# Performance work log

Hardware: AMD Instinct MI355X
Metric: run time of the kernel (lower is better)

Reference implementation:

```python
import jax, jax.numpy as jnp
import numpy as np

G = 64          # grid_size
BC = 16         # base_channels
LATENT = 128

def _conv3d_s2(x, w, b):
    # x: [B,C,D,H,W], w: [O,I,3,3,3], stride 2, pad 1
    y = jax.lax.conv_general_dilated(
        x, w, window_strides=(2, 2, 2), padding=((1, 1), (1, 1), (1, 1)),
        dimension_numbers=('NCDHW', 'OIDHW', 'NCDHW'))
    return y + b[None, :, None, None, None]

def setup_inputs() -> dict:
    key = jax.random.key(0)
    ks = jax.random.split(key, 9)
    B, N = 32, 16384
    partial_coords = jax.random.uniform(ks[0], (B, N, 3), jnp.float32, -1.0, 1.0)
    def he(k, shape, fan_in):
        return jax.random.normal(k, shape, jnp.float32) * np.float32(np.sqrt(2.0 / fan_in))
    w1 = he(ks[1], (BC, 1, 3, 3, 3), 1 * 27)
    b1 = jnp.zeros((BC,), jnp.float32)
    w2 = he(ks[2], (2 * BC, BC, 3, 3, 3), BC * 27)
    b2 = jnp.zeros((2 * BC,), jnp.float32)
    w3 = he(ks[3], (4 * BC, 2 * BC, 3, 3, 3), 2 * BC * 27)
    b3 = jnp.zeros((4 * BC,), jnp.float32)
    fc_in = 4 * BC * (G // 8) ** 3
    fc_w = he(ks[4], (LATENT, fc_in), fc_in)
    fc_b = jnp.zeros((LATENT,), jnp.float32)
    return {'partial_coords': partial_coords, 'w1': w1, 'b1': b1, 'w2': w2,
            'b2': b2, 'w3': w3, 'b3': b3, 'fc_w': fc_w, 'fc_b': fc_b}

def reference(partial_coords, w1, b1, w2, b2, w3, b3, fc_w, fc_b):
    B, N, _ = partial_coords.shape
    # voxelize: scale [-1,1] -> [0, G-1], truncate (matches torch .long()), clamp
    coords_scaled = (partial_coords + 1.0) * 0.5 * (G - 1)
    ci = jnp.clip(coords_scaled.astype(jnp.int32), 0, G - 1)  # [B,N,3] = (x,y,z)
    bidx = jnp.broadcast_to(jnp.arange(B, dtype=jnp.int32)[:, None], (B, N))
    grid = jnp.zeros((B, G, G, G), jnp.float32)
    # grid[b, z, y, x] = 1.0  (single vectorized scatter)
    grid = grid.at[bidx, ci[..., 2], ci[..., 1], ci[..., 0]].set(1.0)
    x = grid[:, None]  # [B,1,G,G,G]
    x = jax.nn.relu(_conv3d_s2(x, w1, b1))
    x = jax.nn.relu(_conv3d_s2(x, w2, b2))
    x = jax.nn.relu(_conv3d_s2(x, w3, b3))  # [B,4*BC,G/8,G/8,G/8]
    feat = x.reshape(B, -1)
    return feat @ fc_w.T + fc_b  # [B,128]
```

## Files before the change

kernel.cpp:

```cpp
#include <hip/hip_runtime.h>
#include <hip/hip_bf16.h>


typedef __attribute__((ext_vector_type(8))) short bf16x8;
typedef __attribute__((ext_vector_type(4))) float f32x4;

__device__ inline unsigned short f2bf(float f) {
    __hip_bfloat16 h = __float2bfloat16(f);
    return *reinterpret_cast<unsigned short*>(&h);
}

__global__ void k_scatter(const float* __restrict__ coords,
                          unsigned char* __restrict__ grid) {
    int i = blockIdx.x * 256 + threadIdx.x;
    float cx = coords[3 * i + 0];
    float cy = coords[3 * i + 1];
    float cz = coords[3 * i + 2];
    int ix = (int)((cx + 1.0f) * 0.5f * 63.0f);
    int iy = (int)((cy + 1.0f) * 0.5f * 63.0f);
    int iz = (int)((cz + 1.0f) * 0.5f * 63.0f);
    ix = min(max(ix, 0), 63);
    iy = min(max(iy, 0), 63);
    iz = min(max(iz, 0), 63);
    int b = i >> 14;
    grid[((b * 64 + iz) * 64 + iy) * 64 + ix] = 1;
}

__global__ __launch_bounds__(256) void k_conv1(
        const unsigned char* __restrict__ grid,
        const float* __restrict__ w1,
        const float* __restrict__ b1,
        unsigned short* __restrict__ c1b) {
    __shared__ float hal[9 * 17 * 20];
    const int t = threadIdx.x;
    const int blk = blockIdx.x;
    const int b = blk >> 7;
    const int zb = (blk >> 4) & 7;
    const int yb = (blk >> 2) & 3;
    const int xb = blk & 3;
    const int iz0 = 8 * zb - 1, iy0 = 16 * yb - 1, ix0 = 16 * xb - 1;

    const unsigned char* g = grid + b * 262144;
    for (int i = t; i < 2601; i += 256) {
        int hz = i / 289, rm = i - hz * 289;
        int hy = rm / 17, hx = rm - hy * 17;
        int iz = iz0 + hz, iy = iy0 + hy, ix = ix0 + hx;
        bool ok = (iz >= 0) & (iy >= 0) & (ix >= 0);
        float v = ok ? (float)g[(iz * 64 + iy) * 64 + ix] : 0.0f;
        int ux = (hx & 1) ? 10 + (hx >> 1) : (hx >> 1);
        hal[(hz * 17 + hy) * 20 + ux] = v;
    }
    __syncthreads();

    const int x = t & 7, y = (t >> 3) & 7, tz = t >> 6;
    const int base = (2 * tz * 17) * 20 + (2 * y) * 20 + x;
    float in27[27];
#pragma unroll
    for (int kz = 0; kz < 3; ++kz)
#pragma unroll
        for (int ky = 0; ky < 3; ++ky)
#pragma unroll
            for (int kx = 0; kx < 3; ++kx) {
                int uxo = (kx == 1) ? 10 : ((kx == 2) ? 1 : 0);
                in27[kz * 9 + ky * 3 + kx] =
                    hal[base + (kz * 17 + ky) * 20 + uxo];
            }
    float r[16];
#pragma unroll
    for (int oc = 0; oc < 16; ++oc) {
        float acc = b1[oc];
#pragma unroll
        for (int k = 0; k < 27; ++k) acc = fmaf(w1[oc * 27 + k], in27[k], acc);
        r[oc] = fmaxf(acc, 0.0f);
    }
    unsigned int dw[8];
#pragma unroll
    for (int j = 0; j < 8; ++j)
        dw[j] = (unsigned int)f2bf(r[2 * j]) | ((unsigned int)f2bf(r[2 * j + 1]) << 16);
    int oz = 4 * zb + tz, oy = 8 * yb + y, ox = 8 * xb + x;
    size_t idx = ((size_t)(b * 32 + oz) * 32 + oy) * 32 + ox;
    char* base_o = (char*)c1b + idx * 32;
    *(int4*)base_o        = int4{(int)dw[0], (int)dw[1], (int)dw[2], (int)dw[3]};
    *(int4*)(base_o + 16) = int4{(int)dw[4], (int)dw[5], (int)dw[6], (int)dw[7]};
}

__global__ void k_wtrans(const float* __restrict__ w2, unsigned short* __restrict__ w2b,
                         const float* __restrict__ w3, unsigned short* __restrict__ w3b) {
    int i = blockIdx.x * 256 + threadIdx.x;
    if (i < 14336) {
        int sh = i >> 9, oc = (i >> 4) & 31, c = i & 15;
        float v = (sh < 27) ? w2[oc * 432 + c * 27 + sh] : 0.0f;
        w2b[i] = f2bf(v);
    } else {
        int j = i - 14336;
        if (j < 55296) {
            int sh = j >> 11, oc = (j >> 5) & 63, c = j & 31;
            w3b[j] = f2bf(w3[oc * 864 + c * 27 + sh]);
        }
    }
}

__device__ constexpr int abase(int sh) {
    return (sh / 9) * 35376 + (((sh % 9) / 3) & 1) * 18224 +
           (((sh % 9) / 3) >> 1) * 1072 + (sh % 3) * 32;
}

__global__ __launch_bounds__(512) void k_conv2_mfma(
        const unsigned short* __restrict__ c1b,
        const unsigned short* __restrict__ w2b,
        const float* __restrict__ b2,
        unsigned short* __restrict__ c2b) {
    __shared__ __align__(16) char smem[106128];
    const int t = threadIdx.x;
    const int b = blockIdx.x >> 4;
    const int zo = blockIdx.x & 15;
    const int lane = t & 63;
    const int wid = t >> 6;

    {
        const int4 z4 = {0, 0, 0, 0};
        if (t < 198) {
            int p = t / 66, r = t % 66;
            int col = r >> 1, h = r & 1;
            *(int4*)(smem + p * 35376 + col * 32 + h * 16) = z4;
        }
        if (t >= 256 && t < 454) {
            int i = t - 256;
            int p = i / 66, r = i % 66;
            int row33 = r >> 1, h = r & 1;
            int off = (row33 < 17) ? row33 * 1072 : 18224 + (row33 - 17) * 1072;
            *(int4*)(smem + p * 35376 + off + h * 16) = z4;
        }
    }

    const char* src = (const char*)c1b + (size_t)b * (32768 * 32);
#pragma unroll
    for (int i = 0; i < 6; ++i) {
        const int p = i >> 1;
        int pos = ((i & 1) << 9) + t;
        int iy = pos >> 5, ix = pos & 31;
        int iz = 2 * zo + p - 1;
        int4 v0 = {0, 0, 0, 0}, v1 = {0, 0, 0, 0};
        if (iz >= 0) {
            const char* gp = src + ((size_t)(iz * 1024 + pos)) * 32;
            v0 = *(const int4*)gp;
            v1 = *(const int4*)(gp + 16);
        }
        int iy_st = iy + 1;
        char* d = smem + p * 35376 + ((iy_st & 1) ? 18224 : 0) + (iy_st >> 1) * 1072 +
                  (ix + 1) * 32;
        *(int4*)d = v0;
        *(int4*)(d + 16) = v1;
    }
    __syncthreads();

    const int y = lane & 15;
    const int g = lane >> 4;
    const int h = g & 1;
    const int s = g >> 1;
    const int laneA = y * 1072 + h * 16;
    const int laneB = (lane & 15) * 32 + h * 16 + s * 1024;
    const int x0 = wid * 2;
    const char* wbase = (const char*)w2b;

    f32x4 acc00 = {0, 0, 0, 0}, acc01 = {0, 0, 0, 0};
    f32x4 acc10 = {0, 0, 0, 0}, acc11 = {0, 0, 0, 0};

#pragma unroll
    for (int sp = 0; sp < 14; ++sp) {
        const int sh0 = 2 * sp;
        const int sh1 = (2 * sp + 1 < 27) ? 2 * sp + 1 : 26;
        const int a0 = abase(sh0);
        const int d01 = abase(sh1) - a0;
        const int addrA = laneA + a0 + (s ? d01 : 0) + x0 * 64;
        bf16x8 A0 = *(const bf16x8*)(smem + addrA);
        bf16x8 A1 = *(const bf16x8*)(smem + addrA + 64);
        const char* wb = wbase + sp * 2048 + laneB;
        bf16x8 B0 = *(const bf16x8*)wb;
        bf16x8 B1 = *(const bf16x8*)(wb + 512);
        acc00 = __builtin_amdgcn_mfma_f32_16x16x32_bf16(A0, B0, acc00, 0, 0, 0);
        acc01 = __builtin_amdgcn_mfma_f32_16x16x32_bf16(A0, B1, acc01, 0, 0, 0);
        acc10 = __builtin_amdgcn_mfma_f32_16x16x32_bf16(A1, B0, acc10, 0, 0, 0);
        acc11 = __builtin_amdgcn_mfma_f32_16x16x32_bf16(A1, B1, acc11, 0, 0, 0);
    }

    __syncthreads();
    float* sOut = (float*)smem;
    {
        int ocl = lane & 15;
        int yb = (lane >> 4) * 4;
#pragma unroll
        for (int r = 0; r < 4; ++r) {
            sOut[ocl * 257        + (yb + r) * 16 + x0    ] = acc00[r];
            sOut[(ocl + 16) * 257 + (yb + r) * 16 + x0    ] = acc01[r];
            sOut[ocl * 257        + (yb + r) * 16 + x0 + 1] = acc10[r];
            sOut[(ocl + 16) * 257 + (yb + r) * 16 + x0 + 1] = acc11[r];
        }
    }
    __syncthreads();
    {
        int m = t >> 1, half = t & 1;
        unsigned int dw[8];
#pragma unroll
        for (int j = 0; j < 8; ++j) {
            int oc0 = half * 16 + 2 * j;
            float v0 = fmaxf(sOut[oc0 * 257 + m] + b2[oc0], 0.0f);
            float v1 = fmaxf(sOut[(oc0 + 1) * 257 + m] + b2[oc0 + 1], 0.0f);
            dw[j] = (unsigned int)f2bf(v0) | ((unsigned int)f2bf(v1) << 16);
        }
        char* dst = (char*)c2b + ((size_t)b * 4096 + zo * 256 + m) * 64 + half * 32;
        *(int4*)dst        = int4{(int)dw[0], (int)dw[1], (int)dw[2], (int)dw[3]};
        *(int4*)(dst + 16) = int4{(int)dw[4], (int)dw[5], (int)dw[6], (int)dw[7]};
    }
}

__global__ __launch_bounds__(512) void k_conv3_mfma(
        const unsigned short* __restrict__ c2b,
        const unsigned short* __restrict__ w3b,
        const float* __restrict__ b3,
        float* __restrict__ feat) {
    __shared__ __align__(16) char smem[55488];
    const int t = threadIdx.x;
    const int b = blockIdx.x >> 3;
    const int zo = blockIdx.x & 7;
    const int lane = t & 63;
    const int wid = t >> 6;

    if (t < 396) {
        int p3 = t / 132, j = t % 132;
        int v = j >> 2, g = j & 3;
        int iy_st = (v < 17) ? 0 : (v - 16);
        int ix_st = (v < 17) ? v : 0;
        int ux = (ix_st & 1) ? 9 + (ix_st >> 1) : (ix_st >> 1);
        int u = (p3 * 17 + iy_st) * 17 + ux;
        *(int4*)(smem + u * 64 + g * 16) = int4{0, 0, 0, 0};
    }

    const char* src = (const char*)c2b + (size_t)b * 262144;
#pragma unroll
    for (int r = 0; r < 6; ++r) {
        int i = r * 512 + t;
        int g = i & 3, vox = i >> 2;
        int kz = vox >> 8, pos = vox & 255;
        int iy = pos >> 4, ix = pos & 15;
        int iz = 2 * zo + kz - 1;
        int4 v = {0, 0, 0, 0};
        if (iz >= 0)
            v = *(const int4*)(src + ((size_t)(iz * 256 + pos)) * 64 + g * 16);
        int ix_st = ix + 1;
        int ux = (ix_st & 1) ? 9 + (ix_st >> 1) : (ix_st >> 1);
        int u = (kz * 17 + iy + 1) * 17 + ux;
        *(int4*)(smem + u * 64 + g * 16) = v;
    }
    __syncthreads();

    const int mt = wid >> 1;
    const int ntp = wid & 1;
    const int m = mt * 16 + (lane & 15);
    const int y = m >> 3, x = m & 7;
    const int g = lane >> 4;
    const int laneA = (34 * y + x) * 64 + g * 16;
    const char* wb_base = (const char*)w3b + (ntp * 32 + (lane & 15)) * 64 + g * 16;

    f32x4 acc0 = {0, 0, 0, 0}, acc1 = {0, 0, 0, 0};

#pragma unroll
    for (int sh = 0; sh < 27; ++sh) {
        const int kz = sh / 9, ky = (sh % 9) / 3, kx = sh % 3;
        const int uxc = (kx == 0) ? 0 : ((kx == 1) ? 9 : 1);
        const int aoff = (289 * kz + 17 * ky + uxc) * 64;
        bf16x8 A = *(const bf16x8*)(smem + laneA + aoff);
        const char* wb = wb_base + sh * 4096;
        bf16x8 B0 = *(const bf16x8*)wb;
        bf16x8 B1 = *(const bf16x8*)(wb + 1024);
        acc0 = __builtin_amdgcn_mfma_f32_16x16x32_bf16(A, B0, acc0, 0, 0, 0);
        acc1 = __builtin_amdgcn_mfma_f32_16x16x32_bf16(A, B1, acc1, 0, 0, 0);
    }

    __syncthreads();
    float* sOut = (float*)smem;
    {
        int ocl = lane & 15;
        int mb = mt * 16 + (lane >> 4) * 4;
#pragma unroll
        for (int r = 0; r < 4; ++r) {
            sOut[(ntp * 32 + ocl) * 65 + mb + r]      = acc0[r];
            sOut[(ntp * 32 + 16 + ocl) * 65 + mb + r] = acc1[r];
        }
    }
    __syncthreads();
    {
        int oc = t >> 3, q = t & 7;
        float bb = b3[oc];
        float* dst = feat + (size_t)b * 32768 + oc * 512 + zo * 64 + q * 8;
#pragma unroll
        for (int k = 0; k < 8; ++k) {
            float v = sOut[oc * 65 + q * 8 + k] + bb;
            dst[k] = fmaxf(v, 0.0f);
        }
    }
}

__global__ void k_fc_partial(const float* __restrict__ feat,
                             const float* __restrict__ fc_w,
                             float* __restrict__ part) {
    __shared__ float lds[256 * 36];
    int fchunk = blockIdx.x & 127;
    int lg = blockIdx.x >> 7;
    int t = threadIdx.x;
    int f0 = fchunk * 256;
    for (int b = 0; b < 32; ++b)
        lds[t * 36 + b] = feat[b * 32768 + f0 + t];
    __syncthreads();

    int l = lg * 32 + (t >> 3);
    int bq = t & 7;
    const float* wrow = fc_w + l * 32768 + f0;
    float a0 = 0.f, a1 = 0.f, a2 = 0.f, a3 = 0.f;
    for (int f = 0; f < 256; ++f) {
        float wv = wrow[f];
        const float* p = &lds[f * 36 + bq * 4];
        a0 = fmaf(p[0], wv, a0);
        a1 = fmaf(p[1], wv, a1);
        a2 = fmaf(p[2], wv, a2);
        a3 = fmaf(p[3], wv, a3);
    }
    int b0 = bq * 4;
    float* pd = part + (size_t)fchunk * 4096 + l;
    pd[(b0 + 0) * 128] = a0;
    pd[(b0 + 1) * 128] = a1;
    pd[(b0 + 2) * 128] = a2;
    pd[(b0 + 3) * 128] = a3;
}

__global__ void k_fc_reduce(const float* __restrict__ part,
                            const float* __restrict__ fc_b,
                            float* __restrict__ out) {
    int idx = blockIdx.x * 256 + threadIdx.x;
    int l = idx & 127;
    float s = fc_b[l];
#pragma unroll 8
    for (int fc = 0; fc < 128; ++fc)
        s += part[fc * 4096 + idx];
    out[idx] = s;
}

extern "C" void kernel_launch(void* const* d_in, const int* in_sizes, int n_in,
                              void* d_out, int out_size, void* d_ws, size_t ws_size,
                              hipStream_t stream) {
    const float* coords = (const float*)d_in[0];
    const float* w1 = (const float*)d_in[1];
    const float* b1 = (const float*)d_in[2];
    const float* w2 = (const float*)d_in[3];
    const float* b2 = (const float*)d_in[4];
    const float* w3 = (const float*)d_in[5];
    const float* b3 = (const float*)d_in[6];
    const float* fc_w = (const float*)d_in[7];
    const float* fc_b = (const float*)d_in[8];

    unsigned char* grid_u8 = (unsigned char*)d_ws;
    unsigned short* w2b = (unsigned short*)((char*)d_ws + 65536);
    unsigned short* w3b = (unsigned short*)((char*)d_ws + 131072);
    unsigned short* c1b = (unsigned short*)((char*)d_ws + 8388608);
    unsigned short* c2b = (unsigned short*)((char*)d_ws + 75497472);
    float* feat = (float*)((char*)d_ws + 92274688);
    float* part = (float*)((char*)d_ws + 96468992);
    float* out = (float*)d_out;

    hipMemsetAsync(grid_u8, 0, 8388608, stream);

    k_scatter<<<2048, 256, 0, stream>>>(coords, grid_u8);
    k_conv1<<<4096, 256, 0, stream>>>(grid_u8, w1, b1, c1b);
    k_wtrans<<<272, 256, 0, stream>>>(w2, w2b, w3, w3b);
    k_conv2_mfma<<<512, 512, 0, stream>>>(c1b, w2b, b2, c2b);
    k_conv3_mfma<<<256, 512, 0, stream>>>(c2b, w3b, b3, feat);
    k_fc_partial<<<512, 256, 0, stream>>>(feat, fc_w, part);
    k_fc_reduce<<<16, 256, 0, stream>>>(part, fc_b, out);
}
```

Measured before the change: 169.2 us.

## Split conv2 blocks in x, fuse weight transform into scatter, vectorize FC loads

Conv2 now gives each block half of the x range. This cuts its LDS footprint roughly in half, doubles the grid to 1024 blocks and sets a launch bound asking for 4 blocks per CU, so more blocks can be resident at once. In exchange, each wave issues only two MFMAs per step, and the output is written in 16-byte pieces. The weight transform kernel is merged into the scatter kernel to remove one launch. The FC partial kernel now reads weights as float4 and unrolls the inner loop by four. The workspace offsets for the converted weights are also moved.

```diff
diff --git a/kernel.cpp b/kernel.cpp
--- a/kernel.cpp
+++ b/kernel.cpp
@@ -10,20 +10,40 @@
     return *reinterpret_cast<unsigned short*>(&h);
 }
 
-__global__ void k_scatter(const float* __restrict__ coords,
-                          unsigned char* __restrict__ grid) {
-    int i = blockIdx.x * 256 + threadIdx.x;
-    float cx = coords[3 * i + 0];
-    float cy = coords[3 * i + 1];
-    float cz = coords[3 * i + 2];
-    int ix = (int)((cx + 1.0f) * 0.5f * 63.0f);
-    int iy = (int)((cy + 1.0f) * 0.5f * 63.0f);
-    int iz = (int)((cz + 1.0f) * 0.5f * 63.0f);
-    ix = min(max(ix, 0), 63);
-    iy = min(max(iy, 0), 63);
-    iz = min(max(iz, 0), 63);
-    int b = i >> 14;
-    grid[((b * 64 + iz) * 64 + iy) * 64 + ix] = 1;
+__global__ void k_scatter_wtrans(const float* __restrict__ coords,
+                                 unsigned char* __restrict__ grid,
+                                 const float* __restrict__ w2,
+                                 unsigned short* __restrict__ w2b,
+                                 const float* __restrict__ w3,
+                                 unsigned short* __restrict__ w3b) {
+    int blk = blockIdx.x;
+    if (blk < 2048) {
+        int i = blk * 256 + threadIdx.x;
+        float cx = coords[3 * i + 0];
+        float cy = coords[3 * i + 1];
+        float cz = coords[3 * i + 2];
+        int ix = (int)((cx + 1.0f) * 0.5f * 63.0f);
+        int iy = (int)((cy + 1.0f) * 0.5f * 63.0f);
+        int iz = (int)((cz + 1.0f) * 0.5f * 63.0f);
+        ix = min(max(ix, 0), 63);
+        iy = min(max(iy, 0), 63);
+        iz = min(max(iz, 0), 63);
+        int b = i >> 14;
+        grid[((b * 64 + iz) * 64 + iy) * 64 + ix] = 1;
+    } else {
+        int i = (blk - 2048) * 256 + threadIdx.x;
+        if (i < 14336) {
+            int sh = i >> 9, oc = (i >> 4) & 31, c = i & 15;
+            float v = (sh < 27) ? w2[oc * 432 + c * 27 + sh] : 0.0f;
+            w2b[i] = f2bf(v);
+        } else {
+            int j = i - 14336;
+            if (j < 55296) {
+                int sh = j >> 11, oc = (j >> 5) & 63, c = j & 31;
+                w3b[j] = f2bf(w3[oc * 864 + c * 27 + sh]);
+            }
+        }
+    }
 }
 
 __global__ __launch_bounds__(256) void k_conv1(
@@ -84,104 +104,66 @@
     *(int4*)(base_o + 16) = int4{(int)dw[4], (int)dw[5], (int)dw[6], (int)dw[7]};
 }
 
-__global__ void k_wtrans(const float* __restrict__ w2, unsigned short* __restrict__ w2b,
-                         const float* __restrict__ w3, unsigned short* __restrict__ w3b) {
-    int i = blockIdx.x * 256 + threadIdx.x;
-    if (i < 14336) {
-        int sh = i >> 9, oc = (i >> 4) & 31, c = i & 15;
-        float v = (sh < 27) ? w2[oc * 432 + c * 27 + sh] : 0.0f;
-        w2b[i] = f2bf(v);
-    } else {
-        int j = i - 14336;
-        if (j < 55296) {
-            int sh = j >> 11, oc = (j >> 5) & 63, c = j & 31;
-            w3b[j] = f2bf(w3[oc * 864 + c * 27 + sh]);
-        }
-    }
-}
-
-__device__ constexpr int abase(int sh) {
-    return (sh / 9) * 35376 + (((sh % 9) / 3) & 1) * 18224 +
-           (((sh % 9) / 3) >> 1) * 1072 + (sh % 3) * 32;
-}
-
-__global__ __launch_bounds__(512) void k_conv2_mfma(
+__device__ constexpr int abase2(int sh) {
+    return (sh / 9) * 18480 + (((sh % 9) / 3) & 1) * 9520 +
+           (((sh % 9) / 3) >> 1) * 560 + (sh % 3) * 32;
+}
+
+__global__ __launch_bounds__(512, 4) void k_conv2_mfma(
         const unsigned short* __restrict__ c1b,
         const unsigned short* __restrict__ w2b,
         const float* __restrict__ b2,
         unsigned short* __restrict__ c2b) {
-    __shared__ __align__(16) char smem[106128];
+    __shared__ __align__(16) char smem[55440];
     const int t = threadIdx.x;
-    const int b = blockIdx.x >> 4;
-    const int zo = blockIdx.x & 15;
+    const int b = blockIdx.x >> 5;
+    const int zo = (blockIdx.x >> 1) & 15;
+    const int xh = blockIdx.x & 1;
     const int lane = t & 63;
     const int wid = t >> 6;
 
-    {
-        const int4 z4 = {0, 0, 0, 0};
-        if (t < 198) {
-            int p = t / 66, r = t % 66;
-            int col = r >> 1, h = r & 1;
-            *(int4*)(smem + p * 35376 + col * 32 + h * 16) = z4;
-        }
-        if (t >= 256 && t < 454) {
-            int i = t - 256;
-            int p = i / 66, r = i % 66;
-            int row33 = r >> 1, h = r & 1;
-            int off = (row33 < 17) ? row33 * 1072 : 18224 + (row33 - 17) * 1072;
-            *(int4*)(smem + p * 35376 + off + h * 16) = z4;
-        }
-    }
-
     const char* src = (const char*)c1b + (size_t)b * (32768 * 32);
-#pragma unroll
-    for (int i = 0; i < 6; ++i) {
-        const int p = i >> 1;
-        int pos = ((i & 1) << 9) + t;
-        int iy = pos >> 5, ix = pos & 31;
-        int iz = 2 * zo + p - 1;
+    for (int i = t; i < 1683; i += 512) {
+        int kz = i / 561, rem = i - kz * 561;
+        int iy_st = rem / 17, c = rem - iy_st * 17;
+        int iz = 2 * zo + kz - 1;
+        int iy = iy_st - 1;
+        int ix = (xh << 4) + c - 1;
         int4 v0 = {0, 0, 0, 0}, v1 = {0, 0, 0, 0};
-        if (iz >= 0) {
-            const char* gp = src + ((size_t)(iz * 1024 + pos)) * 32;
+        if ((iz >= 0) & (iy >= 0) & (ix >= 0)) {
+            const char* gp = src + ((size_t)((iz * 32 + iy) * 32 + ix)) * 32;
             v0 = *(const int4*)gp;
             v1 = *(const int4*)(gp + 16);
         }
-        int iy_st = iy + 1;
-        char* d = smem + p * 35376 + ((iy_st & 1) ? 18224 : 0) + (iy_st >> 1) * 1072 +
-                  (ix + 1) * 32;
+        char* d = smem + kz * 18480 + (iy_st & 1) * 9520 + (iy_st >> 1) * 560 + c * 32;
         *(int4*)d = v0;
         *(int4*)(d + 16) = v1;
     }
     __syncthreads();
 
-    const int y = lane & 15;
+    const int y16 = lane & 15;
     const int g = lane >> 4;
     const int h = g & 1;
     const int s = g >> 1;
-    const int laneA = y * 1072 + h * 16;
+    const int laneA = y16 * 560 + h * 16;
     const int laneB = (lane & 15) * 32 + h * 16 + s * 1024;
-    const int x0 = wid * 2;
+    const int xl64 = wid * 64;
     const char* wbase = (const char*)w2b;
 
-    f32x4 acc00 = {0, 0, 0, 0}, acc01 = {0, 0, 0, 0};
-    f32x4 acc10 = {0, 0, 0, 0}, acc11 = {0, 0, 0, 0};
+    f32x4 acc0 = {0, 0, 0, 0}, acc1 = {0, 0, 0, 0};
 
 #pragma unroll
     for (int sp = 0; sp < 14; ++sp) {
         const int sh0 = 2 * sp;
         const int sh1 = (2 * sp + 1 < 27) ? 2 * sp + 1 : 26;
-        const int a0 = abase(sh0);
-        const int d01 = abase(sh1) - a0;
-        const int addrA = laneA + a0 + (s ? d01 : 0) + x0 * 64;
-        bf16x8 A0 = *(const bf16x8*)(smem + addrA);
-        bf16x8 A1 = *(const bf16x8*)(smem + addrA + 64);
+        const int a0 = abase2(sh0);
+        const int d01 = abase2(sh1) - a0;
+        bf16x8 A = *(const bf16x8*)(smem + laneA + a0 + (s ? d01 : 0) + xl64);
         const char* wb = wbase + sp * 2048 + laneB;
         bf16x8 B0 = *(const bf16x8*)wb;
         bf16x8 B1 = *(const bf16x8*)(wb + 512);
-        acc00 = __builtin_amdgcn_mfma_f32_16x16x32_bf16(A0, B0, acc00, 0, 0, 0);
-        acc01 = __builtin_amdgcn_mfma_f32_16x16x32_bf16(A0, B1, acc01, 0, 0, 0);
-        acc10 = __builtin_amdgcn_mfma_f32_16x16x32_bf16(A1, B0, acc10, 0, 0, 0);
-        acc11 = __builtin_amdgcn_mfma_f32_16x16x32_bf16(A1, B1, acc11, 0, 0, 0);
+        acc0 = __builtin_amdgcn_mfma_f32_16x16x32_bf16(A, B0, acc0, 0, 0, 0);
+        acc1 = __builtin_amdgcn_mfma_f32_16x16x32_bf16(A, B1, acc1, 0, 0, 0);
     }
 
     __syncthreads();
@@ -191,26 +173,25 @@
         int yb = (lane >> 4) * 4;
 #pragma unroll
         for (int r = 0; r < 4; ++r) {
-            sOut[ocl * 257        + (yb + r) * 16 + x0    ] = acc00[r];
-            sOut[(ocl + 16) * 257 + (yb + r) * 16 + x0    ] = acc01[r];
-            sOut[ocl * 257        + (yb + r) * 16 + x0 + 1] = acc10[r];
-            sOut[(ocl + 16) * 257 + (yb + r) * 16 + x0 + 1] = acc11[r];
+            sOut[ocl * 129        + (yb + r) * 8 + wid] = acc0[r];
+            sOut[(ocl + 16) * 129 + (yb + r) * 8 + wid] = acc1[r];
         }
     }
     __syncthreads();
     {
-        int m = t >> 1, half = t & 1;
-        unsigned int dw[8];
-#pragma unroll
-        for (int j = 0; j < 8; ++j) {
-            int oc0 = half * 16 + 2 * j;
-            float v0 = fmaxf(sOut[oc0 * 257 + m] + b2[oc0], 0.0f);
-            float v1 = fmaxf(sOut[(oc0 + 1) * 257 + m] + b2[oc0 + 1], 0.0f);
+        int vox = t >> 2, q = t & 3;
+        unsigned int dw[4];
+#pragma unroll
+        for (int j = 0; j < 4; ++j) {
+            int oc0 = 8 * q + 2 * j;
+            float v0 = fmaxf(sOut[oc0 * 129 + vox] + b2[oc0], 0.0f);
+            float v1 = fmaxf(sOut[(oc0 + 1) * 129 + vox] + b2[oc0 + 1], 0.0f);
             dw[j] = (unsigned int)f2bf(v0) | ((unsigned int)f2bf(v1) << 16);
         }
-        char* dst = (char*)c2b + ((size_t)b * 4096 + zo * 256 + m) * 64 + half * 32;
-        *(int4*)dst        = int4{(int)dw[0], (int)dw[1], (int)dw[2], (int)dw[3]};
-        *(int4*)(dst + 16) = int4{(int)dw[4], (int)dw[5], (int)dw[6], (int)dw[7]};
+        char* dst = (char*)c2b +
+                    ((size_t)b * 4096 + zo * 256 + (vox >> 3) * 16 + xh * 8 + (vox & 7)) * 64 +
+                    q * 16;
+        *(int4*)dst = int4{(int)dw[0], (int)dw[1], (int)dw[2], (int)dw[3]};
     }
 }
 
@@ -317,13 +298,20 @@
     int bq = t & 7;
     const float* wrow = fc_w + l * 32768 + f0;
     float a0 = 0.f, a1 = 0.f, a2 = 0.f, a3 = 0.f;
-    for (int f = 0; f < 256; ++f) {
-        float wv = wrow[f];
-        const float* p = &lds[f * 36 + bq * 4];
-        a0 = fmaf(p[0], wv, a0);
-        a1 = fmaf(p[1], wv, a1);
-        a2 = fmaf(p[2], wv, a2);
-        a3 = fmaf(p[3], wv, a3);
+    for (int f4 = 0; f4 < 64; ++f4) {
+        float4 w4 = *(const float4*)(wrow + f4 * 4);
+        const float* p = &lds[(f4 * 4) * 36 + bq * 4];
+        a0 = fmaf(p[0], w4.x, a0); a1 = fmaf(p[1], w4.x, a1);
+        a2 = fmaf(p[2], w4.x, a2); a3 = fmaf(p[3], w4.x, a3);
+        p += 36;
+        a0 = fmaf(p[0], w4.y, a0); a1 = fmaf(p[1], w4.y, a1);
+        a2 = fmaf(p[2], w4.y, a2); a3 = fmaf(p[3], w4.y, a3);
+        p += 36;
+        a0 = fmaf(p[0], w4.z, a0); a1 = fmaf(p[1], w4.z, a1);
+        a2 = fmaf(p[2], w4.z, a2); a3 = fmaf(p[3], w4.z, a3);
+        p += 36;
+        a0 = fmaf(p[0], w4.w, a0); a1 = fmaf(p[1], w4.w, a1);
+        a2 = fmaf(p[2], w4.w, a2); a3 = fmaf(p[3], w4.w, a3);
     }
     int b0 = bq * 4;
     float* pd = part + (size_t)fchunk * 4096 + l;
@@ -359,20 +347,19 @@
     const float* fc_b = (const float*)d_in[8];
 
     unsigned char* grid_u8 = (unsigned char*)d_ws;
-    unsigned short* w2b = (unsigned short*)((char*)d_ws + 65536);
-    unsigned short* w3b = (unsigned short*)((char*)d_ws + 131072);
     unsigned short* c1b = (unsigned short*)((char*)d_ws + 8388608);
     unsigned short* c2b = (unsigned short*)((char*)d_ws + 75497472);
     float* feat = (float*)((char*)d_ws + 92274688);
     float* part = (float*)((char*)d_ws + 96468992);
+    unsigned short* w2b = (unsigned short*)((char*)d_ws + 98566144);
+    unsigned short* w3b = (unsigned short*)((char*)d_ws + 98697216);
     float* out = (float*)d_out;
 
     hipMemsetAsync(grid_u8, 0, 8388608, stream);
 
-    k_scatter<<<2048, 256, 0, stream>>>(coords, grid_u8);
+    k_scatter_wtrans<<<2320, 256, 0, stream>>>(coords, grid_u8, w2, w2b, w3, w3b);
     k_conv1<<<4096, 256, 0, stream>>>(grid_u8, w1, b1, c1b);
-    k_wtrans<<<272, 256, 0, stream>>>(w2, w2b, w3, w3b);
-    k_conv2_mfma<<<512, 512, 0, stream>>>(c1b, w2b, b2, c2b);
+    k_conv2_mfma<<<1024, 512, 0, stream>>>(c1b, w2b, b2, c2b);
     k_conv3_mfma<<<256, 512, 0, stream>>>(c2b, w3b, b3, feat);
     k_fc_partial<<<512, 256, 0, stream>>>(feat, fc_w, part);
     k_fc_reduce<<<16, 256, 0, stream>>>(part, fc_b, out);
```

Result: faster. 163.6 us (-3.3%).
